# Optimization experiments

Measured on AMD Instinct MI355X. Metric: run time of the kernel, lower is better.

The kernel has to match this reference:

```python
import jax, jax.numpy as jnp
import numpy as np

MV = 16  # multivector dimension of the Clifford algebra (Cl(1,3))

def setup_inputs() -> dict:
    key = jax.random.key(0)
    k1, k2, k3 = jax.random.split(key, 3)
    gp = jax.random.normal(k1, (MV, MV, MV), dtype=jnp.float32)  # Cayley table [i,j,k]
    x = jax.random.normal(k2, (2048, 256, MV), dtype=jnp.float32)  # [a,b,j]
    y = jax.random.normal(k3, (2048, 256, MV), dtype=jnp.float32)  # [a,b,k]
    return {"gp": gp, "x": x, "y": y}

def reference(gp, x, y):
    # Original: out1 = einsum('ijk,abj->abik', gp, x); out = einsum('abik,abk->abi', out1, y)
    # Fused into a single contraction (identical math, avoids the [a,b,i,k] intermediate):
    return jnp.einsum('ijk,abj,abk->abi', gp, x, y)
```

## Files before the change

kernel.cpp:

```cpp
#include <hip/hip_runtime.h>

#define MV 16

typedef __attribute__((ext_vector_type(8))) short short8;
typedef __attribute__((ext_vector_type(4))) float f32x4;

template <int TPWAVE>
__global__ __launch_bounds__(256, 4) void gp_pipe_kernel(
    const float* __restrict__ gp,
    const float* __restrict__ x,
    const float* __restrict__ y,
    float* __restrict__ out)
{
    __shared__ unsigned short ldsb[4096];

    const int tid  = threadIdx.x;
    const int lane = tid & 63;
    const int wid  = tid >> 6;
    const int g    = lane >> 4;
    const int p    = lane & 15;
    const int ja   = g >> 1;
    const int kb   = g & 1;

    const float4* gsrc = reinterpret_cast<const float4*>(gp) + tid * 4;
    float4 g0 = gsrc[0], g1 = gsrc[1], g2 = gsrc[2], g3 = gsrc[3];

    const int   tile0 = (blockIdx.x * 4 + wid) * TPWAVE;
    const size_t xoff = (size_t)p * MV + 8 * ja;
    const size_t yoff = (size_t)p * MV + 8 * kb;

    float4 fx0[2][2], fx1[2][2], fy0[2][2], fy1[2][2];

#define LOADTILE(B, T, TILE)                                                   \
    do {                                                                       \
        const float* xp_ = x + (size_t)(TILE) * 16 * MV + xoff;                \
        const float* yp_ = y + (size_t)(TILE) * 16 * MV + yoff;                \
        fx0[B][T] = *reinterpret_cast<const float4*>(xp_);                     \
        fx1[B][T] = *reinterpret_cast<const float4*>(xp_ + 4);                 \
        fy0[B][T] = *reinterpret_cast<const float4*>(yp_);                     \
        fy1[B][T] = *reinterpret_cast<const float4*>(yp_ + 4);                 \
    } while (0)

    LOADTILE(0, 0, tile0 + 0);
    LOADTILE(0, 1, tile0 + 1);

    {
        float gf[16] = {g0.x, g0.y, g0.z, g0.w, g1.x, g1.y, g1.z, g1.w,
                        g2.x, g2.y, g2.z, g2.w, g3.x, g3.y, g3.z, g3.w};
        short8 lo, hi;
        #pragma unroll
        for (int e = 0; e < 8; ++e) {
            __bf16 hl = (__bf16)gf[e];
            __bf16 hh = (__bf16)gf[e + 8];
            lo[e] = __builtin_bit_cast(short, hl);
            hi[e] = __builtin_bit_cast(short, hh);
        }
        const int i = tid >> 4, j = tid & 15;
        const int c = j & 7, jaw = j >> 3;
        unsigned short* d0 = ldsb + ((c * 64 + 32 * jaw) + i) * 8;
        *reinterpret_cast<short8*>(d0)       = lo;
        *reinterpret_cast<short8*>(d0 + 128) = hi;
    }
    __syncthreads();

    short8 bfrag[8];
    #pragma unroll
    for (int c = 0; c < 8; ++c)
        bfrag[c] = *reinterpret_cast<const short8*>(ldsb + (c * 64 + lane) * 8);

    constexpr int P = TPWAVE / 2;
    #pragma unroll
    for (int s = 0; s < P; ++s) {
        const int cur = s & 1, nxt = cur ^ 1;

        if (s + 1 < P) {
            LOADTILE(nxt, 0, tile0 + 2 * (s + 1) + 0);
            LOADTILE(nxt, 1, tile0 + 2 * (s + 1) + 1);
        }

        #pragma unroll
        for (int tt = 0; tt < 2; ++tt) {
            const int tile = tile0 + 2 * s + tt;
            float xs[8] = {fx0[cur][tt].x, fx0[cur][tt].y, fx0[cur][tt].z, fx0[cur][tt].w,
                           fx1[cur][tt].x, fx1[cur][tt].y, fx1[cur][tt].z, fx1[cur][tt].w};
            float ys[8] = {fy0[cur][tt].x, fy0[cur][tt].y, fy0[cur][tt].z, fy0[cur][tt].w,
                           fy1[cur][tt].x, fy1[cur][tt].y, fy1[cur][tt].z, fy1[cur][tt].w};

            f32x4 acc = {0.f, 0.f, 0.f, 0.f};
            #pragma unroll
            for (int c = 0; c < 8; ++c) {
                float xj = xs[c];
                short8 a;
                #pragma unroll
                for (int e = 0; e < 8; ++e) {
                    __bf16 h = (__bf16)(xj * ys[e]);
                    a[e] = __builtin_bit_cast(short, h);
                }
                acc = __builtin_amdgcn_mfma_f32_16x16x32_bf16(a, bfrag[c], acc, 0, 0, 0);
            }

            float* op = out + ((size_t)tile * 16 + 4 * g) * MV + p;
            op[0 * MV] = acc[0];
            op[1 * MV] = acc[1];
            op[2 * MV] = acc[2];
            op[3 * MV] = acc[3];
        }
    }
#undef LOADTILE
}

template <int TPW>
__global__ __launch_bounds__(256) void gp_fused_kernel(
    const float* __restrict__ gp,
    const float* __restrict__ x,
    const float* __restrict__ y,
    float* __restrict__ out,
    int ntiles)
{
    __shared__ unsigned short ldsb[4096];

    const int tid  = threadIdx.x;
    const int lane = tid & 63;
    const int wid  = tid >> 6;
    const int g    = lane >> 4;
    const int p    = lane & 15;
    const int ja   = g >> 1;
    const int kb   = g & 1;

    const float4* gsrc = reinterpret_cast<const float4*>(gp) + tid * 4;
    float4 g0 = gsrc[0], g1 = gsrc[1], g2 = gsrc[2], g3 = gsrc[3];

    const int tile0 = (blockIdx.x * 4 + wid) * TPW;
    const size_t xoff = (size_t)p * MV + 8 * ja;
    const size_t yoff = (size_t)p * MV + 8 * kb;

    float4 xa[TPW][2], ya[TPW][2];
    #pragma unroll
    for (int t = 0; t < TPW; ++t) {
        if (tile0 + t < ntiles) {
            const float* xp = x + (size_t)(tile0 + t) * 16 * MV + xoff;
            const float* yp = y + (size_t)(tile0 + t) * 16 * MV + yoff;
            xa[t][0] = *reinterpret_cast<const float4*>(xp);
            xa[t][1] = *reinterpret_cast<const float4*>(xp + 4);
            ya[t][0] = *reinterpret_cast<const float4*>(yp);
            ya[t][1] = *reinterpret_cast<const float4*>(yp + 4);
        }
    }

    {
        float gf[16] = {g0.x, g0.y, g0.z, g0.w, g1.x, g1.y, g1.z, g1.w,
                        g2.x, g2.y, g2.z, g2.w, g3.x, g3.y, g3.z, g3.w};
        short8 lo, hi;
        #pragma unroll
        for (int e = 0; e < 8; ++e) {
            __bf16 hl = (__bf16)gf[e];
            __bf16 hh = (__bf16)gf[e + 8];
            lo[e] = __builtin_bit_cast(short, hl);
            hi[e] = __builtin_bit_cast(short, hh);
        }
        const int i = tid >> 4, j = tid & 15;
        const int c = j & 7, jaw = j >> 3;
        unsigned short* d0 = ldsb + ((c * 64 + 32 * jaw) + i) * 8;
        *reinterpret_cast<short8*>(d0)       = lo;
        *reinterpret_cast<short8*>(d0 + 128) = hi;
    }
    __syncthreads();

    short8 bfrag[8];
    #pragma unroll
    for (int c = 0; c < 8; ++c)
        bfrag[c] = *reinterpret_cast<const short8*>(ldsb + (c * 64 + lane) * 8);

    #pragma unroll
    for (int t = 0; t < TPW; ++t) {
        if (tile0 + t >= ntiles) continue;

        float xs[8] = {xa[t][0].x, xa[t][0].y, xa[t][0].z, xa[t][0].w,
                       xa[t][1].x, xa[t][1].y, xa[t][1].z, xa[t][1].w};
        float ys[8] = {ya[t][0].x, ya[t][0].y, ya[t][0].z, ya[t][0].w,
                       ya[t][1].x, ya[t][1].y, ya[t][1].z, ya[t][1].w};

        f32x4 acc = {0.f, 0.f, 0.f, 0.f};
        #pragma unroll
        for (int c = 0; c < 8; ++c) {
            float xj = xs[c];
            short8 a;
            #pragma unroll
            for (int e = 0; e < 8; ++e) {
                __bf16 h = (__bf16)(xj * ys[e]);
                a[e] = __builtin_bit_cast(short, h);
            }
            acc = __builtin_amdgcn_mfma_f32_16x16x32_bf16(a, bfrag[c], acc, 0, 0, 0);
        }

        float* op = out + ((size_t)(tile0 + t) * 16 + 4 * g) * MV + p;
        op[0 * MV] = acc[0];
        op[1 * MV] = acc[1];
        op[2 * MV] = acc[2];
        op[3 * MV] = acc[3];
    }
}

__global__ __launch_bounds__(256) void gp_fp32_kernel(
    const float* __restrict__ g,
    const float* __restrict__ x,
    const float* __restrict__ y,
    float* __restrict__ out,
    int npix)
{
    int idx = blockIdx.x * blockDim.x + threadIdx.x;
    if (idx >= npix) return;

    const float4* xv = reinterpret_cast<const float4*>(x) + (size_t)idx * 4;
    const float4* yv = reinterpret_cast<const float4*>(y) + (size_t)idx * 4;

    float xr[MV], yr[MV], acc[MV];
    #pragma unroll
    for (int q = 0; q < 4; ++q) {
        float4 t = xv[q];
        xr[4*q+0] = t.x; xr[4*q+1] = t.y; xr[4*q+2] = t.z; xr[4*q+3] = t.w;
        float4 u = yv[q];
        yr[4*q+0] = u.x; yr[4*q+1] = u.y; yr[4*q+2] = u.z; yr[4*q+3] = u.w;
    }
    #pragma unroll
    for (int i = 0; i < MV; ++i) acc[i] = 0.0f;

    #pragma unroll
    for (int j = 0; j < MV; ++j) {
        #pragma unroll
        for (int k = 0; k < MV; ++k) {
            float pr = xr[j] * yr[k];
            #pragma unroll
            for (int i = 0; i < MV; ++i)
                acc[i] = fmaf(g[(i * MV + j) * MV + k], pr, acc[i]);
        }
    }

    float4* ov = reinterpret_cast<float4*>(out) + (size_t)idx * 4;
    #pragma unroll
    for (int q = 0; q < 4; ++q)
        ov[q] = make_float4(acc[4*q+0], acc[4*q+1], acc[4*q+2], acc[4*q+3]);
}

extern "C" void kernel_launch(void* const* d_in, const int* in_sizes, int n_in,
                              void* d_out, int out_size, void* d_ws, size_t ws_size,
                              hipStream_t stream) {
    const float* gp = (const float*)d_in[0];
    const float* x  = (const float*)d_in[1];
    const float* y  = (const float*)d_in[2];
    float* out      = (float*)d_out;

    int npix = in_sizes[1] / MV;
    constexpr int TPWAVE = 8;

    if ((npix % 16) == 0) {
        int ntiles = npix / 16;
        if (ntiles % (4 * TPWAVE) == 0) {
            int blocks = ntiles / (4 * TPWAVE);
            gp_pipe_kernel<TPWAVE><<<blocks, 256, 0, stream>>>(gp, x, y, out);
        } else {
            constexpr int TPW = 4;
            int blocks = (ntiles + 4 * TPW - 1) / (4 * TPW);
            gp_fused_kernel<TPW><<<blocks, 256, 0, stream>>>(gp, x, y, out, ntiles);
        }
    } else {
        int blocks = (npix + 255) / 256;
        gp_fp32_kernel<<<blocks, 256, 0, stream>>>(gp, x, y, out, npix);
    }
}
```

Measured before the change: 21.17 us.

## Raise occupancy by reading B fragments from LDS per use and single-tile prefetch

Doubles the launch-bounds occupancy target to 8 blocks per CU. To cut register pressure, it reads the Cayley-table B fragments from LDS inside the MFMA loop instead of keeping eight short8 in registers. It also prefetches one tile ahead rather than two, switches to 32-bit unsigned offset math, and halves tiles per wave to 4, which doubles the block count. The aim is better latency hiding for the memory-bound stream, at the cost of repeated LDS reads and less in-flight prefetch per wave.

```diff
diff --git a/kernel.cpp b/kernel.cpp
--- a/kernel.cpp
+++ b/kernel.cpp
@@ -6,7 +6,7 @@
 typedef __attribute__((ext_vector_type(4))) float f32x4;
 
 template <int TPWAVE>
-__global__ __launch_bounds__(256, 4) void gp_pipe_kernel(
+__global__ __launch_bounds__(256, 8) void gp_hiocc_kernel(
     const float* __restrict__ gp,
     const float* __restrict__ x,
     const float* __restrict__ y,
@@ -19,30 +19,27 @@
     const int wid  = tid >> 6;
     const int g    = lane >> 4;
     const int p    = lane & 15;
-    const int ja   = g >> 1;
-    const int kb   = g & 1;
 
     const float4* gsrc = reinterpret_cast<const float4*>(gp) + tid * 4;
     float4 g0 = gsrc[0], g1 = gsrc[1], g2 = gsrc[2], g3 = gsrc[3];
 
-    const int   tile0 = (blockIdx.x * 4 + wid) * TPWAVE;
-    const size_t xoff = (size_t)p * MV + 8 * ja;
-    const size_t yoff = (size_t)p * MV + 8 * kb;
-
-    float4 fx0[2][2], fx1[2][2], fy0[2][2], fy1[2][2];
-
-#define LOADTILE(B, T, TILE)                                                   \
+    const int tile0 = (blockIdx.x * 4 + wid) * TPWAVE;
+    const unsigned xoff = (unsigned)p * MV + 8u * (unsigned)(g >> 1);
+    const unsigned yoff = (unsigned)p * MV + 8u * (unsigned)(g & 1);
+
+    float4 bx0[2], bx1[2], by0[2], by1[2];
+
+#define LOADTILE(S, TILE)                                                      \
     do {                                                                       \
-        const float* xp_ = x + (size_t)(TILE) * 16 * MV + xoff;                \
-        const float* yp_ = y + (size_t)(TILE) * 16 * MV + yoff;                \
-        fx0[B][T] = *reinterpret_cast<const float4*>(xp_);                     \
-        fx1[B][T] = *reinterpret_cast<const float4*>(xp_ + 4);                 \
-        fy0[B][T] = *reinterpret_cast<const float4*>(yp_);                     \
-        fy1[B][T] = *reinterpret_cast<const float4*>(yp_ + 4);                 \
+        const float* xp_ = x + (unsigned)(TILE) * 256u + xoff;                 \
+        const float* yp_ = y + (unsigned)(TILE) * 256u + yoff;                 \
+        bx0[S] = *reinterpret_cast<const float4*>(xp_);                        \
+        bx1[S] = *reinterpret_cast<const float4*>(xp_ + 4);                    \
+        by0[S] = *reinterpret_cast<const float4*>(yp_);                        \
+        by1[S] = *reinterpret_cast<const float4*>(yp_ + 4);                    \
     } while (0)
 
-    LOADTILE(0, 0, tile0 + 0);
-    LOADTILE(0, 1, tile0 + 1);
+    LOADTILE(0, tile0);
 
     {
         float gf[16] = {g0.x, g0.y, g0.z, g0.w, g1.x, g1.y, g1.z, g1.w,
@@ -63,48 +60,41 @@
     }
     __syncthreads();
 
-    short8 bfrag[8];
-    #pragma unroll
-    for (int c = 0; c < 8; ++c)
-        bfrag[c] = *reinterpret_cast<const short8*>(ldsb + (c * 64 + lane) * 8);
-
-    constexpr int P = TPWAVE / 2;
-    #pragma unroll
-    for (int s = 0; s < P; ++s) {
-        const int cur = s & 1, nxt = cur ^ 1;
-
-        if (s + 1 < P) {
-            LOADTILE(nxt, 0, tile0 + 2 * (s + 1) + 0);
-            LOADTILE(nxt, 1, tile0 + 2 * (s + 1) + 1);
-        }
-
-        #pragma unroll
-        for (int tt = 0; tt < 2; ++tt) {
-            const int tile = tile0 + 2 * s + tt;
-            float xs[8] = {fx0[cur][tt].x, fx0[cur][tt].y, fx0[cur][tt].z, fx0[cur][tt].w,
-                           fx1[cur][tt].x, fx1[cur][tt].y, fx1[cur][tt].z, fx1[cur][tt].w};
-            float ys[8] = {fy0[cur][tt].x, fy0[cur][tt].y, fy0[cur][tt].z, fy0[cur][tt].w,
-                           fy1[cur][tt].x, fy1[cur][tt].y, fy1[cur][tt].z, fy1[cur][tt].w};
-
-            f32x4 acc = {0.f, 0.f, 0.f, 0.f};
+    const unsigned short* bbase = ldsb + (unsigned)lane * 8;
+
+    #pragma unroll
+    for (int t = 0; t < TPWAVE; ++t) {
+        const int cur = t & 1;
+
+        if (t + 1 < TPWAVE) {
+            const int nxt = cur ^ 1;
+            LOADTILE(nxt, tile0 + t + 1);
+        }
+
+        float xs[8] = {bx0[cur].x, bx0[cur].y, bx0[cur].z, bx0[cur].w,
+                       bx1[cur].x, bx1[cur].y, bx1[cur].z, bx1[cur].w};
+        float ys[8] = {by0[cur].x, by0[cur].y, by0[cur].z, by0[cur].w,
+                       by1[cur].x, by1[cur].y, by1[cur].z, by1[cur].w};
+
+        f32x4 acc = {0.f, 0.f, 0.f, 0.f};
+        #pragma unroll
+        for (int c = 0; c < 8; ++c) {
+            short8 b = *reinterpret_cast<const short8*>(bbase + (unsigned)c * 512);
+            float xj = xs[c];
+            short8 a;
             #pragma unroll
-            for (int c = 0; c < 8; ++c) {
-                float xj = xs[c];
-                short8 a;
-                #pragma unroll
-                for (int e = 0; e < 8; ++e) {
-                    __bf16 h = (__bf16)(xj * ys[e]);
-                    a[e] = __builtin_bit_cast(short, h);
-                }
-                acc = __builtin_amdgcn_mfma_f32_16x16x32_bf16(a, bfrag[c], acc, 0, 0, 0);
+            for (int e = 0; e < 8; ++e) {
+                __bf16 h = (__bf16)(xj * ys[e]);
+                a[e] = __builtin_bit_cast(short, h);
             }
-
-            float* op = out + ((size_t)tile * 16 + 4 * g) * MV + p;
-            op[0 * MV] = acc[0];
-            op[1 * MV] = acc[1];
-            op[2 * MV] = acc[2];
-            op[3 * MV] = acc[3];
-        }
+            acc = __builtin_amdgcn_mfma_f32_16x16x32_bf16(a, b, acc, 0, 0, 0);
+        }
+
+        float* op = out + ((unsigned)(tile0 + t) * 16u + 4u * (unsigned)g) * MV + p;
+        op[0 * MV] = acc[0];
+        op[1 * MV] = acc[1];
+        op[2 * MV] = acc[2];
+        op[3 * MV] = acc[3];
     }
 #undef LOADTILE
 }
@@ -251,13 +241,13 @@
     float* out      = (float*)d_out;
 
     int npix = in_sizes[1] / MV;
-    constexpr int TPWAVE = 8;
+    constexpr int TPWAVE = 4;
 
     if ((npix % 16) == 0) {
         int ntiles = npix / 16;
         if (ntiles % (4 * TPWAVE) == 0) {
             int blocks = ntiles / (4 * TPWAVE);
-            gp_pipe_kernel<TPWAVE><<<blocks, 256, 0, stream>>>(gp, x, y, out);
+            gp_hiocc_kernel<TPWAVE><<<blocks, 256, 0, stream>>>(gp, x, y, out);
         } else {
             constexpr int TPW = 4;
             int blocks = (ntiles + 4 * TPW - 1) / (4 * TPW);
```

New measurement: 29.25 us. 38.2% more time.
